# Optimization experiments

Hardware: AMD Instinct MI355X
Metric: run time of the kernel (lower is better)

Reference implementation:

```python
import jax, jax.numpy as jnp
import numpy as np

N_NODES = 100000
N_HID = 128
N_ETYPES = 10
N_EDGES = 100000  # edges per etype


def setup_inputs() -> dict:
    key = jax.random.key(0)
    k1, k2, k3, k4 = jax.random.split(key, 4)
    h = jax.random.normal(k1, (N_NODES, N_HID), dtype=jnp.float32)
    W = jax.random.normal(k2, (N_ETYPES, N_HID), dtype=jnp.float32)
    src = jax.random.randint(k3, (N_ETYPES, N_EDGES), 0, N_NODES, dtype=jnp.int64)
    dst = jax.random.randint(k4, (N_ETYPES, N_EDGES), 0, N_NODES, dtype=jnp.int64)
    rel = jnp.arange(N_ETYPES, dtype=jnp.int64)  # rel2idx: etype -> relation row
    return {"h": h, "W": W, "src": src, "dst": dst, "rel": rel}


def reference(h, W, src, dst, rel):
    # DistMult: score(e) = sum_d h[src_e, d] * W[rel_e, d] * h[dst_e, d]
    h_u = h[src]          # [T, E, d]  gather src features
    h_v = h[dst]          # [T, E, d]  gather dst features
    h_r = W[rel]          # [T, d]     relation embedding per etype
    scores = jnp.einsum('ted,td,ted->te', h_u, h_r, h_v)  # [T, E]
    # pretrain_mode path applies sigmoid per etype
    return jax.nn.sigmoid(scores)
```

## Files before the change

kernel.cpp:

```cpp
#include <hip/hip_runtime.h>
#include <hip/hip_fp16.h>
#include <math.h>

#define N_NODES  100000
#define N_HID    128
#define N_ETYPES 10
#define N_EDGES  100000

#define EDGES_PER_HW 4

typedef __attribute__((ext_vector_type(2))) _Float16 h2v;

#if defined(__has_builtin)
#if __has_builtin(__builtin_amdgcn_fdot2)
#define HAVE_FDOT2 1
#endif
#endif

__device__ __forceinline__ float dot2acc(h2v a, h2v b, float c) {
#ifdef HAVE_FDOT2
    return __builtin_amdgcn_fdot2(a, b, c, false);
#else
    return c + (float)a.x * (float)b.x + (float)a.y * (float)b.y;
#endif
}

template<int CTRL>
__device__ __forceinline__ float ror_add(float p) {
    int r = __builtin_amdgcn_update_dpp(0, __float_as_int(p), CTRL, 0xF, 0xF, true);
    return p + __int_as_float(r);
}

__device__ __forceinline__ float row16_sum(float p) {
    p = ror_add<0x121>(p);
    p = ror_add<0x122>(p);
    p = ror_add<0x124>(p);
    p = ror_add<0x128>(p);
    return p;
}

__global__ __launch_bounds__(256) void convert_kernel(
    const float* __restrict__ h, const float* __restrict__ W,
    __half* __restrict__ h16, __half* __restrict__ W16)
{
    const size_t i = ((size_t)blockIdx.x * 256 + threadIdx.x) * 8;
    const float4 f0 = *(const float4*)(h + i);
    const float4 f1 = *(const float4*)(h + i + 4);
    union { uint4 u; __half2 p[4]; } pk;
    pk.p[0] = __floats2half2_rn(f0.x, f0.y);
    pk.p[1] = __floats2half2_rn(f0.z, f0.w);
    pk.p[2] = __floats2half2_rn(f1.x, f1.y);
    pk.p[3] = __floats2half2_rn(f1.z, f1.w);
    *(uint4*)(h16 + i) = pk.u;

    if (blockIdx.x == 0 && threadIdx.x < (N_ETYPES * N_HID / 8)) {
        const size_t j = (size_t)threadIdx.x * 8;
        const float4 g0 = *(const float4*)(W + j);
        const float4 g1 = *(const float4*)(W + j + 4);
        union { uint4 u; __half2 p[4]; } pw;
        pw.p[0] = __floats2half2_rn(g0.x, g0.y);
        pw.p[1] = __floats2half2_rn(g0.z, g0.w);
        pw.p[2] = __floats2half2_rn(g1.x, g1.y);
        pw.p[3] = __floats2half2_rn(g1.z, g1.w);
        *(uint4*)(W16 + j) = pw.u;
    }
}

__device__ __forceinline__ float dot_row(uint4 a, uint4 b, const h2v uwp[4]) {
    union { uint4 u; h2v p[4]; } ua, ub;
    ua.u = a; ub.u = b;
    float p = dot2acc(ua.p[0], (h2v)(uwp[0] * ub.p[0]), 0.0f);
    p = dot2acc(ua.p[1], (h2v)(uwp[1] * ub.p[1]), p);
    p = dot2acc(ua.p[2], (h2v)(uwp[2] * ub.p[2]), p);
    p = dot2acc(ua.p[3], (h2v)(uwp[3] * ub.p[3]), p);
    return p;
}

__global__ __launch_bounds__(256) void distmult_score_f16_kernel(
    const __half* __restrict__ h16,
    const __half* __restrict__ W16,
    const int*    __restrict__ src,
    const int*    __restrict__ dst,
    const int*    __restrict__ rel,
    float*        __restrict__ out)
{
    const int t    = blockIdx.y;
    const int lane = threadIdx.x & 63;
    const int g    = lane >> 4;
    const int gl   = lane & 15;
    const int wid  = threadIdx.x >> 6;

    const int r = rel[t];
    union { uint4 u; h2v p[4]; } uw;
    uw.u = ((const uint4*)(W16 + (size_t)r * N_HID))[gl];

    const int base = t * N_EDGES;
    const int e0   = (blockIdx.x * 4 + wid) * 8;

    const int* sp = src + base + e0 + g;
    const int* dp = dst + base + e0 + g;
    const int s0 = __builtin_nontemporal_load(sp);
    const int s1 = __builtin_nontemporal_load(sp + 4);
    const int d0 = __builtin_nontemporal_load(dp);
    const int d1 = __builtin_nontemporal_load(dp + 4);

    const unsigned col = (unsigned)gl << 3;
    const uint4 A0 = *(const uint4*)(h16 + (((unsigned)s0 << 7) + col));
    const uint4 B0 = *(const uint4*)(h16 + (((unsigned)d0 << 7) + col));
    const uint4 A1 = *(const uint4*)(h16 + (((unsigned)s1 << 7) + col));
    const uint4 B1 = *(const uint4*)(h16 + (((unsigned)d1 << 7) + col));

    float p0 = dot_row(A0, B0, uw.p);
    float p1 = dot_row(A1, B1, uw.p);

    p0 = row16_sum(p0);
    p1 = row16_sum(p1);

    if (gl < 2) {
        const float res = gl ? p1 : p0;
        const int e = e0 + g + (gl << 2);
        const float sig = 1.0f / (1.0f + __expf(-res));
        __builtin_nontemporal_store(sig, out + base + e);
    }
}

__global__ __launch_bounds__(256) void distmult_score_f32_kernel(
    const float* __restrict__ h,
    const float* __restrict__ W,
    const int*   __restrict__ src,
    const int*   __restrict__ dst,
    const int*   __restrict__ rel,
    float*       __restrict__ out)
{
    const int t    = blockIdx.y;
    const int lane = threadIdx.x & 31;
    const int hw   = (blockIdx.x << 3) + (threadIdx.x >> 5);
    const int r = rel[t];
    const float4 w4 = ((const float4*)(W + (size_t)r * N_HID))[lane];
    const long base = (long)t * N_EDGES;
    const int  e0   = hw * EDGES_PER_HW;

    float res = 0.0f;
    #pragma unroll
    for (int k = 0; k < EDGES_PER_HW; ++k) {
        const int e = e0 + k;
        const int s = src[base + e];
        const int d = dst[base + e];
        const float4 a = ((const float4*)(h + (size_t)s * N_HID))[lane];
        const float4 b = ((const float4*)(h + (size_t)d * N_HID))[lane];
        float p = a.x * w4.x * b.x + a.y * w4.y * b.y
                + a.z * w4.z * b.z + a.w * w4.w * b.w;
        p += __shfl_xor(p, 16, 64);
        p += __shfl_xor(p, 8, 64);
        p += __shfl_xor(p, 4, 64);
        p += __shfl_xor(p, 2, 64);
        p += __shfl_xor(p, 1, 64);
        if (lane == k) res = p;
    }
    if (lane < EDGES_PER_HW) {
        out[base + e0 + lane] = 1.0f / (1.0f + __expf(-res));
    }
}

extern "C" void kernel_launch(void* const* d_in, const int* in_sizes, int n_in,
                              void* d_out, int out_size, void* d_ws, size_t ws_size,
                              hipStream_t stream) {
    const float* h   = (const float*)d_in[0];
    const float* W   = (const float*)d_in[1];
    const int*   src = (const int*)d_in[2];
    const int*   dst = (const int*)d_in[3];
    const int*   rel = (const int*)d_in[4];
    float*       out = (float*)d_out;

    const size_t h16_elems = (size_t)N_NODES * N_HID;
    const size_t need = (h16_elems + N_ETYPES * N_HID) * sizeof(__half);

    dim3 grid(N_EDGES / 32, N_ETYPES);
    dim3 block(256);

    if (ws_size >= need) {
        __half* h16 = (__half*)d_ws;
        __half* W16 = h16 + h16_elems;
        convert_kernel<<<(int)(h16_elems / (256 * 8)), 256, 0, stream>>>(h, W, h16, W16);
        distmult_score_f16_kernel<<<grid, block, 0, stream>>>(h16, W16, src, dst, rel, out);
    } else {
        distmult_score_f32_kernel<<<grid, block, 0, stream>>>(h, W, src, dst, rel, out);
    }
}
```

Measured before the change: 153.5 us.

## Bucket-sort edges by source node to improve gather locality

```diff
diff --git a/kernel.cpp b/kernel.cpp
--- a/kernel.cpp
+++ b/kernel.cpp
@@ -6,6 +6,10 @@
 #define N_HID    128
 #define N_ETYPES 10
 #define N_EDGES  100000
+#define TOT_EDGES (N_ETYPES * N_EDGES)
+
+#define NB       3125
+#define CPAD     16
 
 #define EDGES_PER_HW 4
 
@@ -30,7 +34,6 @@
     int r = __builtin_amdgcn_update_dpp(0, __float_as_int(p), CTRL, 0xF, 0xF, true);
     return p + __int_as_float(r);
 }
-
 __device__ __forceinline__ float row16_sum(float p) {
     p = ror_add<0x121>(p);
     p = ror_add<0x122>(p);
@@ -39,9 +42,21 @@
     return p;
 }
 
+__device__ __forceinline__ float dot_row(uint4 a, uint4 b, uint4 w) {
+    union { uint4 u; h2v p[4]; } ua, ub, uw;
+    ua.u = a; ub.u = b; uw.u = w;
+    float p = dot2acc(ua.p[0], (h2v)(uw.p[0] * ub.p[0]), 0.0f);
+    p = dot2acc(ua.p[1], (h2v)(uw.p[1] * ub.p[1]), p);
+    p = dot2acc(ua.p[2], (h2v)(uw.p[2] * ub.p[2]), p);
+    p = dot2acc(ua.p[3], (h2v)(uw.p[3] * ub.p[3]), p);
+    return p;
+}
+
 __global__ __launch_bounds__(256) void convert_kernel(
     const float* __restrict__ h, const float* __restrict__ W,
-    __half* __restrict__ h16, __half* __restrict__ W16)
+    const int*   __restrict__ rel,
+    __half* __restrict__ h16, __half* __restrict__ Wr16,
+    int* __restrict__ hist)
 {
     const size_t i = ((size_t)blockIdx.x * 256 + threadIdx.x) * 8;
     const float4 f0 = *(const float4*)(h + i);
@@ -53,6 +68,153 @@
     pk.p[3] = __floats2half2_rn(f1.z, f1.w);
     *(uint4*)(h16 + i) = pk.u;
 
+    if (blockIdx.x < 50) {
+        int* p = hist + blockIdx.x * 1024;
+        for (int k = threadIdx.x; k < 1024; k += 256) p[k] = 0;
+    }
+
+    if (blockIdx.x == 0 && threadIdx.x < (N_ETYPES * N_HID / 8)) {
+        const int j = threadIdx.x * 8;
+        const int t = j >> 7;
+        const int c = j & (N_HID - 1);
+        const int r = rel[t];
+        const float4 g0 = *(const float4*)(W + (size_t)r * N_HID + c);
+        const float4 g1 = *(const float4*)(W + (size_t)r * N_HID + c + 4);
+        union { uint4 u; __half2 p[4]; } pw;
+        pw.p[0] = __floats2half2_rn(g0.x, g0.y);
+        pw.p[1] = __floats2half2_rn(g0.z, g0.w);
+        pw.p[2] = __floats2half2_rn(g1.x, g1.y);
+        pw.p[3] = __floats2half2_rn(g1.z, g1.w);
+        *(uint4*)(Wr16 + j) = pw.u;
+    }
+}
+
+__global__ __launch_bounds__(256) void hist_kernel(
+    const int* __restrict__ src, int* __restrict__ hist)
+{
+    const int e0 = (blockIdx.x * 256 + threadIdx.x) * 8;
+    if (e0 >= TOT_EDGES) return;
+    const int4 a = *(const int4*)(src + e0);
+    const int4 b = *(const int4*)(src + e0 + 4);
+    atomicAdd(&hist[(a.x >> 5) * CPAD], 1);
+    atomicAdd(&hist[(a.y >> 5) * CPAD], 1);
+    atomicAdd(&hist[(a.z >> 5) * CPAD], 1);
+    atomicAdd(&hist[(a.w >> 5) * CPAD], 1);
+    atomicAdd(&hist[(b.x >> 5) * CPAD], 1);
+    atomicAdd(&hist[(b.y >> 5) * CPAD], 1);
+    atomicAdd(&hist[(b.z >> 5) * CPAD], 1);
+    atomicAdd(&hist[(b.w >> 5) * CPAD], 1);
+}
+
+__global__ __launch_bounds__(1024) void scan_kernel(
+    const int* __restrict__ hist, int* __restrict__ cursor)
+{
+    __shared__ int lds[1024];
+    const int t = threadIdx.x;
+    int v[4]; int s = 0;
+    #pragma unroll
+    for (int k = 0; k < 4; ++k) {
+        const int i = t * 4 + k;
+        v[k] = (i < NB) ? hist[i * CPAD] : 0;
+        s += v[k];
+    }
+    lds[t] = s;
+    for (int o = 1; o < 1024; o <<= 1) {
+        __syncthreads();
+        const int x = (t >= o) ? lds[t - o] : 0;
+        __syncthreads();
+        lds[t] += x;
+    }
+    int excl = lds[t] - s;
+    #pragma unroll
+    for (int k = 0; k < 4; ++k) {
+        const int i = t * 4 + k;
+        if (i < NB) { cursor[i * CPAD] = excl; excl += v[k]; }
+    }
+}
+
+__global__ __launch_bounds__(256) void scatter_kernel(
+    const int* __restrict__ src, const int* __restrict__ dst,
+    int* __restrict__ cursor, uint2* __restrict__ rec)
+{
+    const int e0 = (blockIdx.x * 256 + threadIdx.x) * 8;
+    if (e0 >= TOT_EDGES) return;
+    const int4 s0 = *(const int4*)(src + e0);
+    const int4 s1 = *(const int4*)(src + e0 + 4);
+    const int4 d0 = *(const int4*)(dst + e0);
+    const int4 d1 = *(const int4*)(dst + e0 + 4);
+    const int ss[8] = { s0.x, s0.y, s0.z, s0.w, s1.x, s1.y, s1.z, s1.w };
+    const int dd[8] = { d0.x, d0.y, d0.z, d0.w, d1.x, d1.y, d1.z, d1.w };
+    #pragma unroll
+    for (int k = 0; k < 8; ++k) {
+        const int e   = e0 + k;
+        const int ety = (int)(((unsigned long long)(unsigned)e * 1407374884ULL) >> 47);
+        const int off = e - ety * N_EDGES;
+        const int pos = atomicAdd(&cursor[(ss[k] >> 5) * CPAD], 1);
+        const unsigned lo = (unsigned)ss[k] | ((unsigned)dd[k] << 17);
+        const unsigned hi = ((unsigned)dd[k] >> 15) | ((unsigned)ety << 2) | ((unsigned)off << 6);
+        rec[pos] = make_uint2(lo, hi);
+    }
+}
+
+__global__ __launch_bounds__(256) void score_kernel(
+    const __half* __restrict__ h16,
+    const __half* __restrict__ Wr16,
+    const uint2*  __restrict__ rec,
+    float*        __restrict__ out)
+{
+    const int lane = threadIdx.x & 63;
+    const int g    = lane >> 4;
+    const int gl   = lane & 15;
+    const int wid  = threadIdx.x >> 6;
+    const int p0i  = blockIdx.x * 32 + wid * 8;
+
+    const uint2 r0 = rec[p0i + g];
+    const uint2 r1 = rec[p0i + 4 + g];
+
+    const unsigned col = (unsigned)gl << 3;
+
+    const unsigned sA = r0.x & 131071u;
+    const unsigned dA = ((r0.x >> 17) | (r0.y << 15)) & 131071u;
+    const unsigned tA = (r0.y >> 2) & 15u;
+    const unsigned oA = (r0.y >> 6) & 131071u;
+    const unsigned sB = r1.x & 131071u;
+    const unsigned dB = ((r1.x >> 17) | (r1.y << 15)) & 131071u;
+    const unsigned tB = (r1.y >> 2) & 15u;
+    const unsigned oB = (r1.y >> 6) & 131071u;
+
+    const uint4 W0 = *(const uint4*)(Wr16 + ((tA << 7) + col));
+    const uint4 W1 = *(const uint4*)(Wr16 + ((tB << 7) + col));
+    const uint4 A0 = *(const uint4*)(h16 + ((sA << 7) + col));
+    const uint4 B0 = *(const uint4*)(h16 + ((dA << 7) + col));
+    const uint4 A1 = *(const uint4*)(h16 + ((sB << 7) + col));
+    const uint4 B1 = *(const uint4*)(h16 + ((dB << 7) + col));
+
+    float p0 = dot_row(A0, B0, W0);
+    float p1 = dot_row(A1, B1, W1);
+    p0 = row16_sum(p0);
+    p1 = row16_sum(p1);
+
+    if (gl < 2) {
+        const float res = gl ? p1 : p0;
+        const int   idx = gl ? (int)(tB * N_EDGES + oB) : (int)(tA * N_EDGES + oA);
+        out[idx] = 1.0f / (1.0f + __expf(-res));
+    }
+}
+
+__global__ __launch_bounds__(256) void convert_legacy_kernel(
+    const float* __restrict__ h, const float* __restrict__ W,
+    __half* __restrict__ h16, __half* __restrict__ W16)
+{
+    const size_t i = ((size_t)blockIdx.x * 256 + threadIdx.x) * 8;
+    const float4 f0 = *(const float4*)(h + i);
+    const float4 f1 = *(const float4*)(h + i + 4);
+    union { uint4 u; __half2 p[4]; } pk;
+    pk.p[0] = __floats2half2_rn(f0.x, f0.y);
+    pk.p[1] = __floats2half2_rn(f0.z, f0.w);
+    pk.p[2] = __floats2half2_rn(f1.x, f1.y);
+    pk.p[3] = __floats2half2_rn(f1.z, f1.w);
+    *(uint4*)(h16 + i) = pk.u;
     if (blockIdx.x == 0 && threadIdx.x < (N_ETYPES * N_HID / 8)) {
         const size_t j = (size_t)threadIdx.x * 8;
         const float4 g0 = *(const float4*)(W + j);
@@ -66,16 +228,6 @@
     }
 }
 
-__device__ __forceinline__ float dot_row(uint4 a, uint4 b, const h2v uwp[4]) {
-    union { uint4 u; h2v p[4]; } ua, ub;
-    ua.u = a; ub.u = b;
-    float p = dot2acc(ua.p[0], (h2v)(uwp[0] * ub.p[0]), 0.0f);
-    p = dot2acc(ua.p[1], (h2v)(uwp[1] * ub.p[1]), p);
-    p = dot2acc(ua.p[2], (h2v)(uwp[2] * ub.p[2]), p);
-    p = dot2acc(ua.p[3], (h2v)(uwp[3] * ub.p[3]), p);
-    return p;
-}
-
 __global__ __launch_bounds__(256) void distmult_score_f16_kernel(
     const __half* __restrict__ h16,
     const __half* __restrict__ W16,
@@ -89,38 +241,27 @@
     const int g    = lane >> 4;
     const int gl   = lane & 15;
     const int wid  = threadIdx.x >> 6;
-
     const int r = rel[t];
     union { uint4 u; h2v p[4]; } uw;
     uw.u = ((const uint4*)(W16 + (size_t)r * N_HID))[gl];
-
     const int base = t * N_EDGES;
     const int e0   = (blockIdx.x * 4 + wid) * 8;
-
     const int* sp = src + base + e0 + g;
     const int* dp = dst + base + e0 + g;
-    const int s0 = __builtin_nontemporal_load(sp);
-    const int s1 = __builtin_nontemporal_load(sp + 4);
-    const int d0 = __builtin_nontemporal_load(dp);
-    const int d1 = __builtin_nontemporal_load(dp + 4);
-
+    const int s0 = sp[0], s1 = sp[4], d0 = dp[0], d1 = dp[4];
     const unsigned col = (unsigned)gl << 3;
     const uint4 A0 = *(const uint4*)(h16 + (((unsigned)s0 << 7) + col));
     const uint4 B0 = *(const uint4*)(h16 + (((unsigned)d0 << 7) + col));
     const uint4 A1 = *(const uint4*)(h16 + (((unsigned)s1 << 7) + col));
     const uint4 B1 = *(const uint4*)(h16 + (((unsigned)d1 << 7) + col));
-
-    float p0 = dot_row(A0, B0, uw.p);
-    float p1 = dot_row(A1, B1, uw.p);
-
+    float p0 = dot_row(A0, B0, uw.u);
+    float p1 = dot_row(A1, B1, uw.u);
     p0 = row16_sum(p0);
     p1 = row16_sum(p1);
-
     if (gl < 2) {
         const float res = gl ? p1 : p0;
         const int e = e0 + g + (gl << 2);
-        const float sig = 1.0f / (1.0f + __expf(-res));
-        __builtin_nontemporal_store(sig, out + base + e);
+        out[base + e] = 1.0f / (1.0f + __expf(-res));
     }
 }
 
@@ -139,7 +280,6 @@
     const float4 w4 = ((const float4*)(W + (size_t)r * N_HID))[lane];
     const long base = (long)t * N_EDGES;
     const int  e0   = hw * EDGES_PER_HW;
-
     float res = 0.0f;
     #pragma unroll
     for (int k = 0; k < EDGES_PER_HW; ++k) {
@@ -172,18 +312,37 @@
     const int*   rel = (const int*)d_in[4];
     float*       out = (float*)d_out;
 
-    const size_t h16_elems = (size_t)N_NODES * N_HID;
-    const size_t need = (h16_elems + N_ETYPES * N_HID) * sizeof(__half);
-
-    dim3 grid(N_EDGES / 32, N_ETYPES);
-    dim3 block(256);
-
-    if (ws_size >= need) {
+    const size_t h16_bytes  = (size_t)N_NODES * N_HID * sizeof(__half);
+    const size_t rec_bytes  = (size_t)TOT_EDGES * 8;
+    const size_t wr16_bytes = 4096;
+    const size_t cnt_bytes  = 51200 * sizeof(int);
+    const size_t need_full  = h16_bytes + rec_bytes + wr16_bytes + 2 * cnt_bytes;
+    const size_t need_f16   = h16_bytes + (size_t)N_ETYPES * N_HID * sizeof(__half);
+
+    if (ws_size >= need_full) {
+        char* w = (char*)d_ws;
+        __half* h16   = (__half*)w;              w += h16_bytes;
+        uint2*  rec   = (uint2*)w;               w += rec_bytes;
+        __half* Wr16  = (__half*)w;              w += wr16_bytes;
+        int*    hist  = (int*)w;                 w += cnt_bytes;
+        int*    cursor= (int*)w;
+
+        convert_kernel<<<(int)(((size_t)N_NODES * N_HID) / (256 * 8)), 256, 0, stream>>>(
+            h, W, rel, h16, Wr16, hist);
+        const int nblk = (TOT_EDGES + 2047) / 2048;
+        hist_kernel<<<nblk, 256, 0, stream>>>(src, hist);
+        scan_kernel<<<1, 1024, 0, stream>>>(hist, cursor);
+        scatter_kernel<<<nblk, 256, 0, stream>>>(src, dst, cursor, rec);
+        score_kernel<<<TOT_EDGES / 32, 256, 0, stream>>>(h16, Wr16, rec, out);
+    } else if (ws_size >= need_f16) {
         __half* h16 = (__half*)d_ws;
-        __half* W16 = h16 + h16_elems;
-        convert_kernel<<<(int)(h16_elems / (256 * 8)), 256, 0, stream>>>(h, W, h16, W16);
-        distmult_score_f16_kernel<<<grid, block, 0, stream>>>(h16, W16, src, dst, rel, out);
+        __half* W16 = h16 + (size_t)N_NODES * N_HID;
+        convert_legacy_kernel<<<(int)(((size_t)N_NODES * N_HID) / (256 * 8)), 256, 0, stream>>>(
+            h, W, h16, W16);
+        dim3 grid(N_EDGES / 32, N_ETYPES);
+        distmult_score_f16_kernel<<<grid, 256, 0, stream>>>(h16, W16, src, dst, rel, out);
     } else {
-        distmult_score_f32_kernel<<<grid, block, 0, stream>>>(h, W, src, dst, rel, out);
-    }
-}
+        dim3 grid(N_EDGES / (8 * EDGES_PER_HW), N_ETYPES);
+        distmult_score_f32_kernel<<<grid, 256, 0, stream>>>(h, W, src, dst, rel, out);
+    }
+}
```

Result: slower. 250.9 us (+63.5%).
